# Performance work log

Hardware: AMD Instinct MI355X
Metric: run time of the kernel (lower is better)

The kernel has to match this reference:

```python
import jax, jax.numpy as jnp
import numpy as np

N_NODES = 50000
N_EDGES = 800000
F_IN = 16
F_EDGE = 8
H = 8  # latent_dim = [8, 8]
NUM_GRAPHS = 512


def setup_inputs() -> dict:
    key = jax.random.key(0)
    ks = jax.random.split(key, 16)
    x = jax.random.normal(ks[0], (N_NODES, F_IN), dtype=jnp.float32)
    edge_index = jax.random.randint(ks[1], (2, N_EDGES), 0, N_NODES)
    edge_attr = jax.random.normal(ks[2], (N_EDGES, F_EDGE), dtype=jnp.float32)
    batch = jnp.sort(jax.random.randint(ks[3], (N_NODES,), 0, NUM_GRAPHS))
    s = 0.1
    # edge MLPs (single Linear each): edge_attr -> flattened [in, out] weight
    We1 = jax.random.normal(ks[4], (F_EDGE, F_IN * H), dtype=jnp.float32) * s
    be1 = jnp.zeros((F_IN * H,), dtype=jnp.float32)
    We2 = jax.random.normal(ks[5], (F_EDGE, H * H), dtype=jnp.float32) * s
    be2 = jnp.zeros((H * H,), dtype=jnp.float32)
    # NNConv root weights + biases
    root1 = jax.random.normal(ks[6], (F_IN, H), dtype=jnp.float32) * s
    b1 = jnp.zeros((H,), dtype=jnp.float32)
    root2 = jax.random.normal(ks[7], (H, H), dtype=jnp.float32) * s
    b2 = jnp.zeros((H,), dtype=jnp.float32)
    # final readout linear H -> 1
    Wlast = jax.random.normal(ks[8], (H, 1), dtype=jnp.float32) * s
    blast = jnp.zeros((1,), dtype=jnp.float32)
    return {"x": x, "edge_index": edge_index, "edge_attr": edge_attr, "batch": batch,
            "We1": We1, "be1": be1, "root1": root1, "b1": b1,
            "We2": We2, "be2": be2, "root2": root2, "b2": b2,
            "Wlast": Wlast, "blast": blast}


def _nnconv(x, src, dst, edge_attr, We, be, root, b, in_dim, out_dim):
    # per-edge weight matrix from edge MLP: [E, in_dim, out_dim]
    W = (edge_attr @ We + be).reshape(-1, in_dim, out_dim)
    # gather source features, per-edge matvec, scatter-add to targets
    msg = jnp.einsum('ei,eio->eo', x[src], W)            # [E, out_dim]
    agg = jax.ops.segment_sum(msg, dst, num_segments=x.shape[0])
    return agg + x @ root + b                            # root weight + bias


def reference(x, edge_index, edge_attr, batch, We1, be1, root1, b1,
              We2, be2, root2, b2, Wlast, blast):
    src, dst = edge_index[0], edge_index[1]
    h = jax.nn.relu(_nnconv(x, src, dst, edge_attr, We1, be1, root1, b1, F_IN, H))
    h = jax.nn.relu(_nnconv(h, src, dst, edge_attr, We2, be2, root2, b2, H, H))
    # per-graph sum pooling (vectorized equivalent of the python loop)
    pooled = jax.ops.segment_sum(h, batch, num_segments=NUM_GRAPHS)  # [G, H]
    return pooled @ Wlast + blast                                    # [G, 1]
```

## Files before the change

kernel.cpp:

```cpp
#include <hip/hip_runtime.h>

#define F_EDGE 8
#define H 8

__device__ __forceinline__ unsigned short f2bf(float f) {
    unsigned u = __float_as_uint(f);
    unsigned r = u + 0x7fffu + ((u >> 16) & 1u);
    return (unsigned short)(r >> 16);
}
__device__ __forceinline__ float bflo(unsigned u) { return __uint_as_float(u << 16); }
__device__ __forceinline__ float bfhi(unsigned u) { return __uint_as_float(u & 0xffff0000u); }

__global__ void init_out_kernel(float* __restrict__ out,
                                const float* __restrict__ blast, int n) {
    int g = blockIdx.x * blockDim.x + threadIdx.x;
    if (g < n) out[g] = blast[0];
}

template <int IN, bool RELU>
__global__ __launch_bounds__(256) void prep_kernel(
    const float* __restrict__ feat,
    const float* __restrict__ We,
    const float* __restrict__ be,
    const float* __restrict__ root,
    const float* __restrict__ b,
    unsigned short* __restrict__ Pt,
    float* __restrict__ q,
    float* __restrict__ aggseed,
    int n_nodes) {
    __shared__ float sW[IN * H * 12];
    int tid = threadIdx.x;
    for (int t = tid; t < IN * H * 12; t += 256) {
        int r = t / 12, m = t - r * 12;
        float v = 0.f;
        if (m < 8) v = We[m * (IN * H) + r];
        else if (m == 8) v = be[r];
        else if (m == 9) v = root[r];
        sW[t] = v;
    }
    __syncthreads();

    int n = blockIdx.x * 32 + (tid >> 3);
    if (n >= n_nodes) return;
    int j = tid & 7;

    float f[IN];
    const float4* fv = (const float4*)(feat + (long long)n * IN);
#pragma unroll
    for (int i4 = 0; i4 < IN / 4; ++i4) {
        float4 v = fv[i4];
        f[i4 * 4 + 0] = v.x; f[i4 * 4 + 1] = v.y;
        f[i4 * 4 + 2] = v.z; f[i4 * 4 + 3] = v.w;
    }
    if (RELU) {
#pragma unroll
        for (int i = 0; i < IN; ++i) f[i] = f[i] > 0.f ? f[i] : 0.f;
    }

    float p[8] = {0.f, 0.f, 0.f, 0.f, 0.f, 0.f, 0.f, 0.f};
    float qq = 0.f, hr = 0.f;
#pragma unroll
    for (int i = 0; i < IN; ++i) {
        const float* row = &sW[(i * 8 + j) * 12];
        float4 w0 = *(const float4*)row;
        float4 w1 = *(const float4*)(row + 4);
        float2 br = *(const float2*)(row + 8);
        float fi = f[i];
        p[0] = fmaf(fi, w0.x, p[0]); p[1] = fmaf(fi, w0.y, p[1]);
        p[2] = fmaf(fi, w0.z, p[2]); p[3] = fmaf(fi, w0.w, p[3]);
        p[4] = fmaf(fi, w1.x, p[4]); p[5] = fmaf(fi, w1.y, p[5]);
        p[6] = fmaf(fi, w1.z, p[6]); p[7] = fmaf(fi, w1.w, p[7]);
        qq = fmaf(fi, br.x, qq);
        hr = fmaf(fi, br.y, hr);
    }
    uint4 pw;
    pw.x = (unsigned)f2bf(p[0]) | ((unsigned)f2bf(p[1]) << 16);
    pw.y = (unsigned)f2bf(p[2]) | ((unsigned)f2bf(p[3]) << 16);
    pw.z = (unsigned)f2bf(p[4]) | ((unsigned)f2bf(p[5]) << 16);
    pw.w = (unsigned)f2bf(p[6]) | ((unsigned)f2bf(p[7]) << 16);
    *(uint4*)(Pt + ((long long)n * H + j) * F_EDGE) = pw;
    q[(long long)n * H + j] = qq;
    aggseed[(long long)n * H + j] = hr + b[j];
}

__global__ __launch_bounds__(256) void edge_fact_kernel(
    const int* __restrict__ ei,
    const float* __restrict__ ea,
    const unsigned short* __restrict__ Pt,
    const float* __restrict__ q,
    float* __restrict__ agg,
    int E) {
    long long gid = (long long)blockIdx.x * blockDim.x + threadIdx.x;
    int e = (int)(gid >> 3);
    if (e >= E) return;
    int j = (int)(gid & 7);

    int src = ei[e];
    int dst = ei[E + e];

    const float4* av = (const float4*)(ea + (long long)e * F_EDGE);
    float4 a0 = av[0], a1 = av[1];

    uint4 pw = *(const uint4*)(Pt + ((long long)src * H + j) * F_EDGE);

    float m = q[(long long)src * H + j];
    m = fmaf(a0.x, bflo(pw.x), m);
    m = fmaf(a0.y, bfhi(pw.x), m);
    m = fmaf(a0.z, bflo(pw.y), m);
    m = fmaf(a0.w, bfhi(pw.y), m);
    m = fmaf(a1.x, bflo(pw.z), m);
    m = fmaf(a1.y, bfhi(pw.z), m);
    m = fmaf(a1.z, bflo(pw.w), m);
    m = fmaf(a1.w, bfhi(pw.w), m);

    unsafeAtomicAdd(&agg[(long long)dst * H + j], m);
}

__global__ __launch_bounds__(256) void pool_kernel(
    const float* __restrict__ h2pre, const int* __restrict__ batch,
    const float* __restrict__ Wlast, float* __restrict__ out,
    int n_nodes, int n_graphs) {
    __shared__ float bins[512];
    bool use_bins = (n_graphs <= 512);
    if (use_bins) {
        for (int t = threadIdx.x; t < n_graphs; t += 256) bins[t] = 0.f;
        __syncthreads();
    }
    float wl[8];
#pragma unroll
    for (int j = 0; j < 8; ++j) wl[j] = Wlast[j];

    int base = blockIdx.x * 1024;
#pragma unroll
    for (int r = 0; r < 4; ++r) {
        int n = base + r * 256 + threadIdx.x;
        if (n < n_nodes) {
            const float4* hv = (const float4*)(h2pre + (long long)n * H);
            float4 h0 = hv[0], h1 = hv[1];
            float c = 0.f;
            c = fmaf(fmaxf(h0.x, 0.f), wl[0], c);
            c = fmaf(fmaxf(h0.y, 0.f), wl[1], c);
            c = fmaf(fmaxf(h0.z, 0.f), wl[2], c);
            c = fmaf(fmaxf(h0.w, 0.f), wl[3], c);
            c = fmaf(fmaxf(h1.x, 0.f), wl[4], c);
            c = fmaf(fmaxf(h1.y, 0.f), wl[5], c);
            c = fmaf(fmaxf(h1.z, 0.f), wl[6], c);
            c = fmaf(fmaxf(h1.w, 0.f), wl[7], c);
            if (use_bins) atomicAdd(&bins[batch[n]], c);
            else unsafeAtomicAdd(&out[batch[n]], c);
        }
    }
    if (use_bins) {
        __syncthreads();
        for (int t = threadIdx.x; t < n_graphs; t += 256) {
            float v = bins[t];
            if (v != 0.f) unsafeAtomicAdd(&out[t], v);
        }
    }
}

extern "C" void kernel_launch(void* const* d_in, const int* in_sizes, int n_in,
                              void* d_out, int out_size, void* d_ws, size_t ws_size,
                              hipStream_t stream) {
    const float* x     = (const float*)d_in[0];
    const int*   ei    = (const int*)d_in[1];
    const float* ea    = (const float*)d_in[2];
    const int*   batch = (const int*)d_in[3];
    const float* We1   = (const float*)d_in[4];
    const float* be1   = (const float*)d_in[5];
    const float* root1 = (const float*)d_in[6];
    const float* b1    = (const float*)d_in[7];
    const float* We2   = (const float*)d_in[8];
    const float* be2   = (const float*)d_in[9];
    const float* root2 = (const float*)d_in[10];
    const float* b2    = (const float*)d_in[11];
    const float* Wlast = (const float*)d_in[12];
    const float* blast = (const float*)d_in[13];
    float* out = (float*)d_out;

    int F_IN_rt = 16;
    int n_nodes = in_sizes[0] / F_IN_rt;
    int E = in_sizes[1] / 2;

    size_t nH = (size_t)n_nodes * H;
    unsigned short* Pt1 = (unsigned short*)d_ws;
    unsigned short* Pt2 = Pt1 + (size_t)n_nodes * H * F_EDGE;
    float* q1    = (float*)(Pt2 + (size_t)n_nodes * H * F_EDGE);
    float* q2    = q1 + nH;
    float* h1pre = q2 + nH;
    float* h2pre = h1pre + nH;

    init_out_kernel<<<(out_size + 255) / 256, 256, 0, stream>>>(out, blast, out_size);

    int nblocks = (n_nodes + 31) / 32;
    prep_kernel<16, false><<<nblocks, 256, 0, stream>>>(
        x, We1, be1, root1, b1, Pt1, q1, h1pre, n_nodes);

    long long lanes = (long long)E * H;
    int eblks = (int)((lanes + 255) / 256);
    edge_fact_kernel<<<eblks, 256, 0, stream>>>(ei, ea, Pt1, q1, h1pre, E);

    prep_kernel<H, true><<<nblocks, 256, 0, stream>>>(
        h1pre, We2, be2, root2, b2, Pt2, q2, h2pre, n_nodes);

    edge_fact_kernel<<<eblks, 256, 0, stream>>>(ei, ea, Pt2, q2, h2pre, E);

    int pblocks = (n_nodes + 1023) / 1024;
    pool_kernel<<<pblocks, 256, 0, stream>>>(h2pre, batch, Wlast, out, n_nodes, out_size);
}
```

Measured before the change: 199.2 us.

## Build per-call CSR by destination and replace atomic scatter with per-node gather

Each call now builds a destination-sorted edge list with a degree count, a single-block scan and an atomic scatter. The two edge kernels then gather per destination node and reduce with wavefront shuffles instead of issuing float atomics for every edge and channel. The second edge pass also applies ReLU, the readout and graph pooling directly, which removes the separate pool kernel; output initialisation moves into the first prep kernel. In exchange there are extra CSR-build kernels each call, a serial single-block scan, and edge-attribute reads that are no longer coalesced because edges are visited in sorted order.

```diff
diff --git a/kernel.cpp b/kernel.cpp
--- a/kernel.cpp
+++ b/kernel.cpp
@@ -11,23 +11,69 @@
 __device__ __forceinline__ float bflo(unsigned u) { return __uint_as_float(u << 16); }
 __device__ __forceinline__ float bfhi(unsigned u) { return __uint_as_float(u & 0xffff0000u); }
 
-__global__ void init_out_kernel(float* __restrict__ out,
-                                const float* __restrict__ blast, int n) {
-    int g = blockIdx.x * blockDim.x + threadIdx.x;
-    if (g < n) out[g] = blast[0];
-}
-
-template <int IN, bool RELU>
+
+__global__ __launch_bounds__(256) void zero_kernel(int* __restrict__ p, int n) {
+    int i = blockIdx.x * 256 + threadIdx.x;
+    if (i < n) p[i] = 0;
+}
+
+__global__ __launch_bounds__(256) void degree_kernel(const int* __restrict__ ei,
+                                                     int* __restrict__ deg, int E) {
+    int e = blockIdx.x * 256 + threadIdx.x;
+    if (e < E) atomicAdd(&deg[ei[E + e]], 1);
+}
+
+__global__ __launch_bounds__(1024) void scan_kernel(const int* __restrict__ deg,
+                                                    int* __restrict__ off,
+                                                    int* __restrict__ cursor, int n) {
+    __shared__ int s[1024];
+    int t = threadIdx.x;
+    int C = (n + 1023) >> 10;
+    int base = t * C;
+    int sum = 0;
+    for (int i = 0; i < C; ++i) {
+        int idx = base + i;
+        if (idx < n) sum += deg[idx];
+    }
+    s[t] = sum;
+    __syncthreads();
+    for (int d = 1; d < 1024; d <<= 1) {
+        int v = (t >= d) ? s[t - d] : 0;
+        __syncthreads();
+        s[t] += v;
+        __syncthreads();
+    }
+    int run = (t == 0) ? 0 : s[t - 1];
+    for (int i = 0; i < C; ++i) {
+        int idx = base + i;
+        if (idx < n) {
+            off[idx] = run;
+            cursor[idx] = run;
+            run += deg[idx];
+        }
+    }
+    if (t == 1023) off[n] = s[1023];
+}
+
+__global__ __launch_bounds__(256) void scatter_kernel(const int* __restrict__ ei,
+                                                      int* __restrict__ cursor,
+                                                      int2* __restrict__ sorted, int E) {
+    int e = blockIdx.x * 256 + threadIdx.x;
+    if (e < E) {
+        int s_ = ei[e];
+        int d_ = ei[E + e];
+        int pos = atomicAdd(&cursor[d_], 1);
+        sorted[pos] = make_int2(s_, e);
+    }
+}
+
+template <int IN, bool RELU, bool INIT>
 __global__ __launch_bounds__(256) void prep_kernel(
-    const float* __restrict__ feat,
-    const float* __restrict__ We,
-    const float* __restrict__ be,
-    const float* __restrict__ root,
-    const float* __restrict__ b,
-    unsigned short* __restrict__ Pt,
-    float* __restrict__ q,
-    float* __restrict__ aggseed,
-    int n_nodes) {
+    const float* __restrict__ feat, const float* __restrict__ We,
+    const float* __restrict__ be, const float* __restrict__ root,
+    const float* __restrict__ b, unsigned short* __restrict__ Pt,
+    float* __restrict__ q, float* __restrict__ aggseed, int n_nodes,
+    float* __restrict__ out, const float* __restrict__ blast, int out_n) {
     __shared__ float sW[IN * H * 12];
     int tid = threadIdx.x;
     for (int t = tid; t < IN * H * 12; t += 256) {
@@ -37,6 +83,10 @@
         else if (m == 8) v = be[r];
         else if (m == 9) v = root[r];
         sW[t] = v;
+    }
+    if (INIT && blockIdx.x == 0) {
+        float bl = blast[0];
+        for (int t = tid; t < out_n; t += 256) out[t] = bl;
     }
     __syncthreads();
 
@@ -83,79 +133,51 @@
     aggseed[(long long)n * H + j] = hr + b[j];
 }
 
-__global__ __launch_bounds__(256) void edge_fact_kernel(
-    const int* __restrict__ ei,
-    const float* __restrict__ ea,
-    const unsigned short* __restrict__ Pt,
-    const float* __restrict__ q,
-    float* __restrict__ agg,
-    int E) {
-    long long gid = (long long)blockIdx.x * blockDim.x + threadIdx.x;
-    int e = (int)(gid >> 3);
-    if (e >= E) return;
-    int j = (int)(gid & 7);
-
-    int src = ei[e];
-    int dst = ei[E + e];
-
-    const float4* av = (const float4*)(ea + (long long)e * F_EDGE);
-    float4 a0 = av[0], a1 = av[1];
-
-    uint4 pw = *(const uint4*)(Pt + ((long long)src * H + j) * F_EDGE);
-
-    float m = q[(long long)src * H + j];
-    m = fmaf(a0.x, bflo(pw.x), m);
-    m = fmaf(a0.y, bfhi(pw.x), m);
-    m = fmaf(a0.z, bflo(pw.y), m);
-    m = fmaf(a0.w, bfhi(pw.y), m);
-    m = fmaf(a1.x, bflo(pw.z), m);
-    m = fmaf(a1.y, bfhi(pw.z), m);
-    m = fmaf(a1.z, bflo(pw.w), m);
-    m = fmaf(a1.w, bfhi(pw.w), m);
-
-    unsafeAtomicAdd(&agg[(long long)dst * H + j], m);
-}
-
-__global__ __launch_bounds__(256) void pool_kernel(
-    const float* __restrict__ h2pre, const int* __restrict__ batch,
-    const float* __restrict__ Wlast, float* __restrict__ out,
-    int n_nodes, int n_graphs) {
-    __shared__ float bins[512];
-    bool use_bins = (n_graphs <= 512);
-    if (use_bins) {
-        for (int t = threadIdx.x; t < n_graphs; t += 256) bins[t] = 0.f;
-        __syncthreads();
-    }
-    float wl[8];
-#pragma unroll
-    for (int j = 0; j < 8; ++j) wl[j] = Wlast[j];
-
-    int base = blockIdx.x * 1024;
-#pragma unroll
-    for (int r = 0; r < 4; ++r) {
-        int n = base + r * 256 + threadIdx.x;
-        if (n < n_nodes) {
-            const float4* hv = (const float4*)(h2pre + (long long)n * H);
-            float4 h0 = hv[0], h1 = hv[1];
-            float c = 0.f;
-            c = fmaf(fmaxf(h0.x, 0.f), wl[0], c);
-            c = fmaf(fmaxf(h0.y, 0.f), wl[1], c);
-            c = fmaf(fmaxf(h0.z, 0.f), wl[2], c);
-            c = fmaf(fmaxf(h0.w, 0.f), wl[3], c);
-            c = fmaf(fmaxf(h1.x, 0.f), wl[4], c);
-            c = fmaf(fmaxf(h1.y, 0.f), wl[5], c);
-            c = fmaf(fmaxf(h1.z, 0.f), wl[6], c);
-            c = fmaf(fmaxf(h1.w, 0.f), wl[7], c);
-            if (use_bins) atomicAdd(&bins[batch[n]], c);
-            else unsafeAtomicAdd(&out[batch[n]], c);
-        }
-    }
-    if (use_bins) {
-        __syncthreads();
-        for (int t = threadIdx.x; t < n_graphs; t += 256) {
-            float v = bins[t];
-            if (v != 0.f) unsafeAtomicAdd(&out[t], v);
-        }
+template <bool FUSE_POOL>
+__global__ __launch_bounds__(256) void edge_csr_kernel(
+    const int* __restrict__ off, const int2* __restrict__ sorted,
+    const float* __restrict__ ea, const unsigned short* __restrict__ Pt,
+    const float* __restrict__ q, const float* __restrict__ seed,
+    float* __restrict__ hout,
+    const int* __restrict__ batch, const float* __restrict__ Wlast,
+    float* __restrict__ out, int n_nodes) {
+    int n = blockIdx.x * 4 + (threadIdx.x >> 6);
+    if (n >= n_nodes) return;
+    int lane = threadIdx.x & 63;
+    int es = lane >> 3, j = lane & 7;
+
+    int start = off[n], end = off[n + 1];
+    float acc = 0.f;
+    for (int k = start + es; k < end; k += 8) {
+        int2 se = sorted[k];
+        const float4* av = (const float4*)(ea + (long long)se.y * F_EDGE);
+        float4 a0 = av[0], a1 = av[1];
+        uint4 pw = *(const uint4*)(Pt + ((long long)se.x * H + j) * F_EDGE);
+        float m = q[(long long)se.x * H + j];
+        m = fmaf(a0.x, bflo(pw.x), m);
+        m = fmaf(a0.y, bfhi(pw.x), m);
+        m = fmaf(a0.z, bflo(pw.y), m);
+        m = fmaf(a0.w, bfhi(pw.y), m);
+        m = fmaf(a1.x, bflo(pw.z), m);
+        m = fmaf(a1.y, bfhi(pw.z), m);
+        m = fmaf(a1.z, bflo(pw.w), m);
+        m = fmaf(a1.w, bfhi(pw.w), m);
+        acc += m;
+    }
+    acc += __shfl_xor(acc, 8);
+    acc += __shfl_xor(acc, 16);
+    acc += __shfl_xor(acc, 32);
+
+    float h = seed[(long long)n * H + j] + acc;
+
+    if (!FUSE_POOL) {
+        if (es == 0) hout[(long long)n * H + j] = h;
+    } else {
+        float c = fmaxf(h, 0.f) * Wlast[j];
+        c += __shfl_xor(c, 1);
+        c += __shfl_xor(c, 2);
+        c += __shfl_xor(c, 4);
+        if (lane == 0) unsafeAtomicAdd(&out[batch[n]], c);
     }
 }
 
@@ -182,29 +204,42 @@
     int n_nodes = in_sizes[0] / F_IN_rt;
     int E = in_sizes[1] / 2;
 
-    size_t nH = (size_t)n_nodes * H;
-    unsigned short* Pt1 = (unsigned short*)d_ws;
-    unsigned short* Pt2 = Pt1 + (size_t)n_nodes * H * F_EDGE;
-    float* q1    = (float*)(Pt2 + (size_t)n_nodes * H * F_EDGE);
-    float* q2    = q1 + nH;
-    float* h1pre = q2 + nH;
-    float* h2pre = h1pre + nH;
-
-    init_out_kernel<<<(out_size + 255) / 256, 256, 0, stream>>>(out, blast, out_size);
+    char* w = (char*)d_ws;
+    auto take = [&](size_t bytes) {
+        char* p = w;
+        w += (bytes + 15) & ~(size_t)15;
+        return p;
+    };
+    unsigned short* Pt1 = (unsigned short*)take((size_t)n_nodes * H * F_EDGE * 2);
+    unsigned short* Pt2 = (unsigned short*)take((size_t)n_nodes * H * F_EDGE * 2);
+    float* q1    = (float*)take((size_t)n_nodes * H * 4);
+    float* q2    = (float*)take((size_t)n_nodes * H * 4);
+    float* h1    = (float*)take((size_t)n_nodes * H * 4);
+    float* h2s   = (float*)take((size_t)n_nodes * H * 4);
+    int* deg     = (int*)take((size_t)n_nodes * 4);
+    int* off     = (int*)take((size_t)(n_nodes + 1) * 4);
+    int* cursor  = (int*)take((size_t)n_nodes * 4);
+    int2* sorted = (int2*)take((size_t)E * 8);
+
+    int nbn = (n_nodes + 255) / 256;
+    int nbe = (E + 255) / 256;
+
+    zero_kernel<<<nbn, 256, 0, stream>>>(deg, n_nodes);
+    degree_kernel<<<nbe, 256, 0, stream>>>(ei, deg, E);
+    scan_kernel<<<1, 1024, 0, stream>>>(deg, off, cursor, n_nodes);
+    scatter_kernel<<<nbe, 256, 0, stream>>>(ei, cursor, sorted, E);
 
     int nblocks = (n_nodes + 31) / 32;
-    prep_kernel<16, false><<<nblocks, 256, 0, stream>>>(
-        x, We1, be1, root1, b1, Pt1, q1, h1pre, n_nodes);
-
-    long long lanes = (long long)E * H;
-    int eblks = (int)((lanes + 255) / 256);
-    edge_fact_kernel<<<eblks, 256, 0, stream>>>(ei, ea, Pt1, q1, h1pre, E);
-
-    prep_kernel<H, true><<<nblocks, 256, 0, stream>>>(
-        h1pre, We2, be2, root2, b2, Pt2, q2, h2pre, n_nodes);
-
-    edge_fact_kernel<<<eblks, 256, 0, stream>>>(ei, ea, Pt2, q2, h2pre, E);
-
-    int pblocks = (n_nodes + 1023) / 1024;
-    pool_kernel<<<pblocks, 256, 0, stream>>>(h2pre, batch, Wlast, out, n_nodes, out_size);
-}
+    prep_kernel<16, false, true><<<nblocks, 256, 0, stream>>>(
+        x, We1, be1, root1, b1, Pt1, q1, h1, n_nodes, out, blast, out_size);
+
+    int ablk = (n_nodes + 3) / 4;
+    edge_csr_kernel<false><<<ablk, 256, 0, stream>>>(
+        off, sorted, ea, Pt1, q1, h1, h1, nullptr, nullptr, nullptr, n_nodes);
+
+    prep_kernel<H, true, false><<<nblocks, 256, 0, stream>>>(
+        h1, We2, be2, root2, b2, Pt2, q2, h2s, n_nodes, nullptr, nullptr, 0);
+
+    edge_csr_kernel<true><<<ablk, 256, 0, stream>>>(
+        off, sorted, ea, Pt2, q2, h2s, nullptr, batch, Wlast, out, n_nodes);
+}
```

Result: slower. 487.7 us (+144.8%).

## Pack edge indices and bf16 edge attributes once, fold output init into prep

Applied to the files above, without the earlier changes.

Adds a pack kernel that interleaves src/dst into int2 and converts edge attributes to bf16. Both edge kernels then read 8-byte index pairs and 16-byte attribute rows instead of two separate index loads plus 32 bytes of fp32 attributes. This cuts per-edge traffic in the two bandwidth-bound scatter passes. The output init kernel is folded into the first prep kernel to save a launch. In exchange it adds an extra full pass over the edge data and rounds edge attributes to bf16, which lowers precision.

```diff
diff --git a/kernel.cpp b/kernel.cpp
--- a/kernel.cpp
+++ b/kernel.cpp
@@ -11,23 +11,29 @@
 __device__ __forceinline__ float bflo(unsigned u) { return __uint_as_float(u << 16); }
 __device__ __forceinline__ float bfhi(unsigned u) { return __uint_as_float(u & 0xffff0000u); }
 
-__global__ void init_out_kernel(float* __restrict__ out,
-                                const float* __restrict__ blast, int n) {
-    int g = blockIdx.x * blockDim.x + threadIdx.x;
-    if (g < n) out[g] = blast[0];
-}
-
-template <int IN, bool RELU>
+__global__ __launch_bounds__(256) void pack_kernel(
+    const int* __restrict__ ei, const float* __restrict__ ea,
+    int2* __restrict__ sd, unsigned short* __restrict__ eab, int E) {
+    int e = blockIdx.x * 256 + threadIdx.x;
+    if (e >= E) return;
+    sd[e] = make_int2(ei[e], ei[E + e]);
+    const float4* av = (const float4*)(ea + (long long)e * F_EDGE);
+    float4 a0 = av[0], a1 = av[1];
+    uint4 pw;
+    pw.x = (unsigned)f2bf(a0.x) | ((unsigned)f2bf(a0.y) << 16);
+    pw.y = (unsigned)f2bf(a0.z) | ((unsigned)f2bf(a0.w) << 16);
+    pw.z = (unsigned)f2bf(a1.x) | ((unsigned)f2bf(a1.y) << 16);
+    pw.w = (unsigned)f2bf(a1.z) | ((unsigned)f2bf(a1.w) << 16);
+    *(uint4*)(eab + (long long)e * F_EDGE) = pw;
+}
+
+template <int IN, bool RELU, bool INIT>
 __global__ __launch_bounds__(256) void prep_kernel(
-    const float* __restrict__ feat,
-    const float* __restrict__ We,
-    const float* __restrict__ be,
-    const float* __restrict__ root,
-    const float* __restrict__ b,
-    unsigned short* __restrict__ Pt,
-    float* __restrict__ q,
-    float* __restrict__ aggseed,
-    int n_nodes) {
+    const float* __restrict__ feat, const float* __restrict__ We,
+    const float* __restrict__ be, const float* __restrict__ root,
+    const float* __restrict__ b, unsigned short* __restrict__ Pt,
+    float* __restrict__ q, float* __restrict__ aggseed, int n_nodes,
+    float* __restrict__ out, const float* __restrict__ blast, int out_n) {
     __shared__ float sW[IN * H * 12];
     int tid = threadIdx.x;
     for (int t = tid; t < IN * H * 12; t += 256) {
@@ -37,6 +43,10 @@
         else if (m == 8) v = be[r];
         else if (m == 9) v = root[r];
         sW[t] = v;
+    }
+    if (INIT && blockIdx.x == 0) {
+        float bl = blast[0];
+        for (int t = tid; t < out_n; t += 256) out[t] = bl;
     }
     __syncthreads();
 
@@ -84,36 +94,29 @@
 }
 
 __global__ __launch_bounds__(256) void edge_fact_kernel(
-    const int* __restrict__ ei,
-    const float* __restrict__ ea,
-    const unsigned short* __restrict__ Pt,
-    const float* __restrict__ q,
-    float* __restrict__ agg,
-    int E) {
-    long long gid = (long long)blockIdx.x * blockDim.x + threadIdx.x;
+    const int2* __restrict__ sd, const unsigned short* __restrict__ eab,
+    const unsigned short* __restrict__ Pt, const float* __restrict__ q,
+    float* __restrict__ agg, int E) {
+    long long gid = (long long)blockIdx.x * 256 + threadIdx.x;
     int e = (int)(gid >> 3);
     if (e >= E) return;
     int j = (int)(gid & 7);
 
-    int src = ei[e];
-    int dst = ei[E + e];
-
-    const float4* av = (const float4*)(ea + (long long)e * F_EDGE);
-    float4 a0 = av[0], a1 = av[1];
-
-    uint4 pw = *(const uint4*)(Pt + ((long long)src * H + j) * F_EDGE);
-
-    float m = q[(long long)src * H + j];
-    m = fmaf(a0.x, bflo(pw.x), m);
-    m = fmaf(a0.y, bfhi(pw.x), m);
-    m = fmaf(a0.z, bflo(pw.y), m);
-    m = fmaf(a0.w, bfhi(pw.y), m);
-    m = fmaf(a1.x, bflo(pw.z), m);
-    m = fmaf(a1.y, bfhi(pw.z), m);
-    m = fmaf(a1.z, bflo(pw.w), m);
-    m = fmaf(a1.w, bfhi(pw.w), m);
-
-    unsafeAtomicAdd(&agg[(long long)dst * H + j], m);
+    int2 se = sd[e];
+    uint4 av = *(const uint4*)(eab + (long long)e * F_EDGE);
+    uint4 pw = *(const uint4*)(Pt + ((long long)se.x * H + j) * F_EDGE);
+    float m = q[(long long)se.x * H + j];
+
+    m = fmaf(bflo(av.x), bflo(pw.x), m);
+    m = fmaf(bfhi(av.x), bfhi(pw.x), m);
+    m = fmaf(bflo(av.y), bflo(pw.y), m);
+    m = fmaf(bfhi(av.y), bfhi(pw.y), m);
+    m = fmaf(bflo(av.z), bflo(pw.z), m);
+    m = fmaf(bfhi(av.z), bfhi(pw.z), m);
+    m = fmaf(bflo(av.w), bflo(pw.w), m);
+    m = fmaf(bfhi(av.w), bfhi(pw.w), m);
+
+    unsafeAtomicAdd(&agg[(long long)se.y * H + j], m);
 }
 
 __global__ __launch_bounds__(256) void pool_kernel(
@@ -182,29 +185,38 @@
     int n_nodes = in_sizes[0] / F_IN_rt;
     int E = in_sizes[1] / 2;
 
-    size_t nH = (size_t)n_nodes * H;
-    unsigned short* Pt1 = (unsigned short*)d_ws;
-    unsigned short* Pt2 = Pt1 + (size_t)n_nodes * H * F_EDGE;
-    float* q1    = (float*)(Pt2 + (size_t)n_nodes * H * F_EDGE);
-    float* q2    = q1 + nH;
-    float* h1pre = q2 + nH;
-    float* h2pre = h1pre + nH;
-
-    init_out_kernel<<<(out_size + 255) / 256, 256, 0, stream>>>(out, blast, out_size);
+    char* w = (char*)d_ws;
+    auto take = [&](size_t bytes) {
+        char* p = w;
+        w += (bytes + 15) & ~(size_t)15;
+        return p;
+    };
+    unsigned short* Pt1 = (unsigned short*)take((size_t)n_nodes * H * F_EDGE * 2);
+    unsigned short* Pt2 = (unsigned short*)take((size_t)n_nodes * H * F_EDGE * 2);
+    float* q1    = (float*)take((size_t)n_nodes * H * 4);
+    float* q2    = (float*)take((size_t)n_nodes * H * 4);
+    float* h1    = (float*)take((size_t)n_nodes * H * 4);
+    float* h2    = (float*)take((size_t)n_nodes * H * 4);
+    int2* sd     = (int2*)take((size_t)E * 8);
+    unsigned short* eab = (unsigned short*)take((size_t)E * F_EDGE * 2);
+
+    int nbe = (E + 255) / 256;
+
+    pack_kernel<<<nbe, 256, 0, stream>>>(ei, ea, sd, eab, E);
 
     int nblocks = (n_nodes + 31) / 32;
-    prep_kernel<16, false><<<nblocks, 256, 0, stream>>>(
-        x, We1, be1, root1, b1, Pt1, q1, h1pre, n_nodes);
+    prep_kernel<16, false, true><<<nblocks, 256, 0, stream>>>(
+        x, We1, be1, root1, b1, Pt1, q1, h1, n_nodes, out, blast, out_size);
 
     long long lanes = (long long)E * H;
     int eblks = (int)((lanes + 255) / 256);
-    edge_fact_kernel<<<eblks, 256, 0, stream>>>(ei, ea, Pt1, q1, h1pre, E);
-
-    prep_kernel<H, true><<<nblocks, 256, 0, stream>>>(
-        h1pre, We2, be2, root2, b2, Pt2, q2, h2pre, n_nodes);
-
-    edge_fact_kernel<<<eblks, 256, 0, stream>>>(ei, ea, Pt2, q2, h2pre, E);
+    edge_fact_kernel<<<eblks, 256, 0, stream>>>(sd, eab, Pt1, q1, h1, E);
+
+    prep_kernel<H, true, false><<<nblocks, 256, 0, stream>>>(
+        h1, We2, be2, root2, b2, Pt2, q2, h2, n_nodes, nullptr, nullptr, 0);
+
+    edge_fact_kernel<<<eblks, 256, 0, stream>>>(sd, eab, Pt2, q2, h2, E);
 
     int pblocks = (n_nodes + 1023) / 1024;
-    pool_kernel<<<pblocks, 256, 0, stream>>>(h2pre, batch, Wlast, out, n_nodes, out_size);
-}
+    pool_kernel<<<pblocks, 256, 0, stream>>>(h2, batch, Wlast, out, n_nodes, out_size);
+}
```

Measured after the change: 204.3 us. 2.5% more time.
